# Performance work log

Hardware: AMD Instinct MI355X
Metric: run time of the kernel (lower is better)

The kernel has to match this reference:

```python
import jax, jax.numpy as jnp
import numpy as np

GRID = (15, 15)
HW = GRID[0] * GRID[1]
IMAGE_SIZE = 240
TEMP = 0.07
EPS = 1e-12


def make_masks(h, w, k):
    grid = np.arange(h * w).reshape(h, w)
    # matches torch unfold: kernel offsets row-major, spatial positions row-major
    idx = np.stack([grid[i:i + h - k + 1, j:j + w - k + 1] for i in range(k) for j in range(k)])
    return jnp.asarray(idx.reshape(k * k, -1), dtype=jnp.int32)  # [k*k, n_masks]


def _l2n(x):
    return x / jnp.maximum(jnp.linalg.norm(x, axis=-1, keepdims=True), EPS)


def cosine_sim(a, b):
    # a: [..., N, D], b: [M, D] -> [..., N, M]
    return jnp.einsum('...nd,md->...nm', _l2n(a), _l2n(b))


def harmonic_aggregation(window_scores, masks):
    # window_scores: [B, n_masks]; masks: [k2, n_masks] flat patch indices
    n_masks = masks.shape[1]
    # membership matrix M[p, w] = 1 if patch p is covered by window w
    M = jnp.zeros((HW, n_masks), dtype=window_scores.dtype)
    M = M.at[masks, jnp.arange(n_masks)[None, :]].set(1.0)
    counts = M.sum(axis=1)                                  # [HW]
    sums = (1.0 / window_scores) @ M.T                      # [B, HW]
    scores = counts[None, :] / sums
    scores = jnp.nan_to_num(scores, nan=0.0, posinf=0.0)
    return scores.reshape(-1, GRID[0], GRID[1])


def visual_association_score(embeds, ref_embeds):
    # embeds: [B, N, D]; ref_embeds: [K, N, D]
    flat = ref_embeds.reshape(-1, embeds.shape[-1])          # [K*N, D]
    scores = cosine_sim(embeds, flat)                        # [B, N, K*N]
    return (1.0 - scores).min(axis=-1) / 2.0                 # [B, N]


def setup_inputs() -> dict:
    key = jax.random.key(0)
    ks = jax.random.split(key, 8)
    B, D, K = 256, 640, 4
    return {
        'image_embeds': jax.random.normal(ks[0], (B, D), jnp.float32),
        'window_embeds_s2': jax.random.normal(ks[1], (B, 196, D), jnp.float32),
        'window_embeds_s3': jax.random.normal(ks[2], (B, 169, D), jnp.float32),
        'patch_embeds': jax.random.normal(ks[3], (B, 225, D), jnp.float32),
        'text_embeds': jax.random.normal(ks[4], (2, D), jnp.float32),
        'ref_patch_embeds': jax.random.normal(ks[5], (K, 225, D), jnp.float32),
        'ref_window_s2': jax.random.normal(ks[6], (K, 196, D), jnp.float32),
        'ref_window_s3': jax.random.normal(ks[7], (K, 169, D), jnp.float32),
        'masks_s2': make_masks(GRID[0], GRID[1], 2),
        'masks_s3': make_masks(GRID[0], GRID[1], 3),
    }


def reference(image_embeds, window_embeds_s2, window_embeds_s3, patch_embeds,
              text_embeds, ref_patch_embeds, ref_window_s2, ref_window_s3,
              masks_s2, masks_s3):
    B = image_embeds.shape[0]
    # image-level zero-shot anomaly score
    img_probs = jax.nn.softmax(cosine_sim(image_embeds, text_embeds) / TEMP, axis=-1)
    image_scores = img_probs[..., 1]                         # [B]

    # zero-shot multi-scale (harmonic mean of image score + window scores)
    zs = [jnp.broadcast_to(image_scores[:, None, None], (B, GRID[0], GRID[1]))]
    for we, m in ((window_embeds_s2, masks_s2), (window_embeds_s3, masks_s3)):
        s = jax.nn.softmax(cosine_sim(we, text_embeds) / TEMP, axis=-1)[..., 1]  # [B, n_masks]
        zs.append(harmonic_aggregation(s, m))
    zero_shot = len(zs) / (1.0 / jnp.stack(zs)).sum(axis=0)   # [B, H, W]

    # few-shot scores
    fs = [visual_association_score(patch_embeds, ref_patch_embeds).reshape(B, GRID[0], GRID[1])]
    for we, re, m in ((window_embeds_s2, ref_window_s2, masks_s2),
                      (window_embeds_s3, ref_window_s3, masks_s3)):
        fs.append(harmonic_aggregation(visual_association_score(we, re), m))
    few_shot = jnp.stack(fs).mean(axis=0)                     # [B, H, W]

    multi_scale = (zero_shot + few_shot) / 2.0
    image_scores = (image_scores + few_shot.max(axis=(-2, -1))) / 2.0
    pixel_scores = jax.image.resize(multi_scale, (B, IMAGE_SIZE, IMAGE_SIZE), method='bilinear')
    return image_scores, pixel_scores
```

## Files before the change

kernel.cpp:

```cpp
#include <hip/hip_runtime.h>
#include <cmath>

#define D 640
#define TEMP_INV (1.0f / 0.07f)

typedef __attribute__((ext_vector_type(8))) short bf16x8;
typedef __attribute__((ext_vector_type(4))) float f32x4;

__device__ __forceinline__ short f2bf(float f) {
    unsigned int u = __float_as_uint(f);
    unsigned int r = (u + 0x7fffu + ((u >> 16) & 1u)) >> 16;
    return (short)r;
}

__device__ __forceinline__ void gload_lds16(const void* g, void* l) {
    __builtin_amdgcn_global_load_lds(
        (const __attribute__((address_space(1))) unsigned int*)g,
        (__attribute__((address_space(3))) unsigned int*)l, 16, 0, 0);
}

__global__ void textnorm_k(const float* __restrict__ T, float* __restrict__ tn) {
    int w = threadIdx.x >> 6, lane = threadIdx.x & 63;
    const float* row = T + w * D;
    float v[10]; float ss = 0.f;
#pragma unroll
    for (int i = 0; i < 10; i++) { v[i] = row[lane + 64 * i]; ss += v[i] * v[i]; }
#pragma unroll
    for (int m = 1; m < 64; m <<= 1) ss += __shfl_xor(ss, m, 64);
    float rn = 1.f / fmaxf(sqrtf(ss), 1e-12f);
#pragma unroll
    for (int i = 0; i < 10; i++) tn[w * D + lane + 64 * i] = v[i] * rn;
}

__global__ __launch_bounds__(256) void normstore_k(
    const float* __restrict__ X, int nsrc, int npad, const float* __restrict__ tn,
    float* __restrict__ score_out, short* __restrict__ bf16_out) {
    int wid = blockIdx.x * 4 + (threadIdx.x >> 6);
    int lane = threadIdx.x & 63;
    if (wid >= npad) return;
    const float2* row = (const float2*)(X + (size_t)(wid < nsrc ? wid : 0) * D);
    const float2* t0 = (const float2*)tn;
    const float2* t1 = (const float2*)(tn + D);
    float2 v[5]; float ss = 0.f, d0 = 0.f, d1 = 0.f;
#pragma unroll
    for (int i = 0; i < 5; i++) {
        float2 a = row[lane + 64 * i];
        v[i] = a;
        ss += a.x * a.x + a.y * a.y;
        if (tn) {
            float2 b0 = t0[lane + 64 * i], b1 = t1[lane + 64 * i];
            d0 += a.x * b0.x + a.y * b0.y;
            d1 += a.x * b1.x + a.y * b1.y;
        }
    }
#pragma unroll
    for (int m = 1; m < 64; m <<= 1) {
        ss += __shfl_xor(ss, m, 64);
        if (tn) { d0 += __shfl_xor(d0, m, 64); d1 += __shfl_xor(d1, m, 64); }
    }
    float rn = 1.f / fmaxf(sqrtf(ss), 1e-12f);
    if (score_out && lane == 0)
        score_out[wid] = 1.f / (1.f + expf(-((d1 - d0) * rn) * TEMP_INV));
    if (bf16_out) {
        ushort2* o = (ushort2*)bf16_out;
#pragma unroll
        for (int i = 0; i < 5; i++) {
            ushort2 p;
            p.x = (unsigned short)f2bf(v[i].x * rn);
            p.y = (unsigned short)f2bf(v[i].y * rn);
            o[(size_t)wid * 320 + lane + 64 * i] = p;
        }
    }
}

__global__ __launch_bounds__(512, 4) void gemm_max_k(
    const short* __restrict__ A, const short* __restrict__ B,
    int nch, int U, float* __restrict__ partial) {
    __shared__ short Al[3][128 * 32];
    __shared__ short Bl[3][256 * 32];
    const int t = threadIdx.x;
    const int g = blockIdx.x & 7, ii = blockIdx.x >> 3;
    const int ulo = (int)(((long long)g * U) >> 3);
    const int uhi = (int)(((long long)(g + 1) * U) >> 3);
    const int u = ulo + ii;
    if (u >= uhi) return;
    const int rc = u / nch, nc = u - rc * nch;
    const int nchq = nch * 4;

    const int srow = t >> 2;
    const int scol = (t & 3) * 16;
    const int gsw = (scol ^ (((t >> 3) & 3) << 4)) >> 1;

    const int lane = t & 63, wave = t >> 6;
    const int l15 = lane & 15, lhi = lane >> 4;
    const int wr = wave >> 2, wc = wave & 3;
    const int kb = (lhi * 16) ^ (((l15 >> 1) & 3) << 4);

    const short* Ag = A + ((size_t)rc * 128 + srow) * D + gsw;
    const short* Bg = B + ((size_t)nc * 256 + srow) * D + gsw;

    auto stage = [&](int buf, int ks) {
        gload_lds16(Ag + ks * 32, (char*)&Al[buf][0] + t * 16);
        gload_lds16(Bg + ks * 32, (char*)&Bl[buf][0] + t * 16);
        gload_lds16(Bg + (size_t)128 * D + ks * 32, (char*)&Bl[buf][0] + 8192 + t * 16);
    };

    f32x4 acc[4][4];
#pragma unroll
    for (int m = 0; m < 4; m++)
#pragma unroll
        for (int n = 0; n < 4; n++) acc[m][n] = (f32x4){0.f, 0.f, 0.f, 0.f};

    stage(0, 0);
    stage(1, 1);

    for (int ks = 0; ks < 20; ks++) {
        asm volatile("s_waitcnt vmcnt(3)" ::: "memory");
        __builtin_amdgcn_s_barrier();
        asm volatile("" ::: "memory");

        int nxt = ks + 2; if (nxt > 19) nxt = 19;
        stage((ks + 2) % 3, nxt);

        const char* Ab = (const char*)&Al[ks % 3][0];
        const char* Bb = (const char*)&Bl[ks % 3][0];
        bf16x8 a[4], b[4];
#pragma unroll
        for (int m = 0; m < 4; m++)
            a[m] = *(const bf16x8*)(Ab + (wr * 64 + m * 16 + l15) * 64 + kb);
#pragma unroll
        for (int n = 0; n < 4; n++)
            b[n] = *(const bf16x8*)(Bb + (wc * 64 + n * 16 + l15) * 64 + kb);
#pragma unroll
        for (int m = 0; m < 4; m++)
#pragma unroll
            for (int n = 0; n < 4; n++)
                acc[m][n] = __builtin_amdgcn_mfma_f32_16x16x32_bf16(a[m], b[n], acc[m][n], 0, 0, 0);
    }

#pragma unroll
    for (int m = 0; m < 4; m++)
#pragma unroll
        for (int r = 0; r < 4; r++) {
            float v = fmaxf(fmaxf(acc[m][0][r], acc[m][1][r]),
                            fmaxf(acc[m][2][r], acc[m][3][r]));
#pragma unroll
            for (int msk = 1; msk < 16; msk <<= 1)
                v = fmaxf(v, __shfl_xor(v, msk, 64));
            if (l15 == 0) {
                int row = rc * 128 + wr * 64 + m * 16 + lhi * 4 + r;
                partial[(size_t)row * nchq + nc * 4 + wc] = v;
            }
        }
}

__global__ __launch_bounds__(256) void reducemax_k(
    const float* __restrict__ partial, int nchq, int nrows, float* __restrict__ vas) {
    int r = blockIdx.x * 256 + threadIdx.x;
    if (r >= nrows) return;
    float m = -1e30f;
    for (int i = 0; i < nchq; i++) m = fmaxf(m, partial[(size_t)r * nchq + i]);
    vas[r] = (1.0f - m) * 0.5f;
}

__global__ __launch_bounds__(256) void rowstats_k(
    const float* __restrict__ X, int nrows, const float* __restrict__ tn,
    float* __restrict__ rnorm_out, float* __restrict__ score_out) {
    int wid = blockIdx.x * 4 + (threadIdx.x >> 6);
    int lane = threadIdx.x & 63;
    if (wid >= nrows) return;
    const float* row = X + (size_t)wid * D;
    float ss = 0.f, d0 = 0.f, d1 = 0.f;
#pragma unroll
    for (int i = 0; i < 10; i++) {
        float v = row[lane + 64 * i];
        ss += v * v;
        if (tn) { d0 += v * tn[lane + 64 * i]; d1 += v * tn[D + lane + 64 * i]; }
    }
#pragma unroll
    for (int m = 1; m < 64; m <<= 1) {
        ss += __shfl_xor(ss, m, 64);
        if (tn) { d0 += __shfl_xor(d0, m, 64); d1 += __shfl_xor(d1, m, 64); }
    }
    if (lane == 0) {
        float rn = 1.f / fmaxf(sqrtf(ss), 1e-12f);
        if (rnorm_out) rnorm_out[wid] = rn;
        if (score_out) score_out[wid] = 1.f / (1.f + expf(-((d1 - d0) * rn) * TEMP_INV));
    }
}

__global__ __launch_bounds__(256) void refnorm_k(
    const float* __restrict__ R, int M, int Mp, short* __restrict__ out) {
    int wid = blockIdx.x * 4 + (threadIdx.x >> 6);
    int lane = threadIdx.x & 63;
    if (wid >= Mp) return;
    const float* row = R + (size_t)(wid < M ? wid : 0) * D;
    float v[10]; float ss = 0.f;
#pragma unroll
    for (int i = 0; i < 10; i++) { v[i] = row[lane + 64 * i]; ss += v[i] * v[i]; }
#pragma unroll
    for (int m = 1; m < 64; m <<= 1) ss += __shfl_xor(ss, m, 64);
    float rn = 1.f / fmaxf(sqrtf(ss), 1e-12f);
#pragma unroll
    for (int i = 0; i < 10; i++) out[(size_t)wid * D + lane + 64 * i] = f2bf(v[i] * rn);
}

#define SA 648
#define SB 72
__global__ __launch_bounds__(256) void maxcos_k(
    const float* __restrict__ X, const float* __restrict__ rnorm,
    const short* __restrict__ refs, int Mp, float* __restrict__ vas_out) {
    __shared__ short Alds[64 * SA];
    __shared__ short Blds[64 * SB];
    const int t = threadIdx.x;
    const size_t rowBase = (size_t)blockIdx.x * 64;
#pragma unroll
    for (int i = 0; i < 20; i++) {
        int c = i * 256 + t;
        int row = c / 80, col = (c % 80) * 8;
        const float* p = X + (rowBase + row) * D + col;
        float rn = rnorm[rowBase + row];
        float4 v0 = *(const float4*)p;
        float4 v1 = *(const float4*)(p + 4);
        bf16x8 s;
        s[0] = f2bf(v0.x * rn); s[1] = f2bf(v0.y * rn);
        s[2] = f2bf(v0.z * rn); s[3] = f2bf(v0.w * rn);
        s[4] = f2bf(v1.x * rn); s[5] = f2bf(v1.y * rn);
        s[6] = f2bf(v1.z * rn); s[7] = f2bf(v1.w * rn);
        *(bf16x8*)&Alds[row * SA + col] = s;
    }
    __syncthreads();
    const int lane = t & 63, wave = t >> 6;
    const int l15 = lane & 15, lhi = lane >> 4;
    const int wr0 = wave * 16;
    float rowmax[4] = {-1e30f, -1e30f, -1e30f, -1e30f};
    for (int m0 = 0; m0 < Mp; m0 += 64) {
        f32x4 zero = {0.f, 0.f, 0.f, 0.f};
        f32x4 acc[4] = {zero, zero, zero, zero};
        for (int ks = 0; ks < 10; ks++) {
            __syncthreads();
#pragma unroll
            for (int c2 = 0; c2 < 2; c2++) {
                int c = c2 * 256 + t;
                int n = c >> 3, kk = (c & 7) * 8;
                const short* g = refs + (size_t)(m0 + n) * D + ks * 64 + kk;
                *(bf16x8*)&Blds[n * SB + kk] = *(const bf16x8*)g;
            }
            __syncthreads();
#pragma unroll
            for (int sub = 0; sub < 2; sub++) {
                bf16x8 a = *(const bf16x8*)&Alds[(wr0 + l15) * SA + ks * 64 + sub * 32 + lhi * 8];
#pragma unroll
                for (int s = 0; s < 4; s++) {
                    bf16x8 b = *(const bf16x8*)&Blds[(s * 16 + l15) * SB + sub * 32 + lhi * 8];
                    acc[s] = __builtin_amdgcn_mfma_f32_16x16x32_bf16(a, b, acc[s], 0, 0, 0);
                }
            }
        }
#pragma unroll
        for (int r = 0; r < 4; r++) {
            float mv = fmaxf(fmaxf(acc[0][r], acc[1][r]), fmaxf(acc[2][r], acc[3][r]));
#pragma unroll
            for (int msk = 1; msk < 16; msk <<= 1) mv = fmaxf(mv, __shfl_xor(mv, msk, 64));
            rowmax[r] = fmaxf(rowmax[r], mv);
        }
    }
    if (l15 == 0) {
#pragma unroll
        for (int r = 0; r < 4; r++) {
            size_t row = rowBase + wr0 + lhi * 4 + r;
            vas_out[row] = (1.0f - rowmax[r]) * 0.5f;
        }
    }
}

__global__ __launch_bounds__(256) void fuse_k(
    const float* __restrict__ imgsc, const float* __restrict__ zs2,
    const float* __restrict__ zs3, const float* __restrict__ vasP,
    const float* __restrict__ vas2, const float* __restrict__ vas3,
    float* __restrict__ multi, float* __restrict__ img_out) {
    int b = blockIdx.x, t = threadIdx.x;
    __shared__ float red[256];
    float few = -1e30f;
    if (t < 225) {
        int i = t / 15, j = t % 15;
        float invz2 = 0.f, invf2 = 0.f; int c2 = 0;
        int ilo = max(0, i - 1), ihi = min(i, 13), jlo = max(0, j - 1), jhi = min(j, 13);
        for (int i0 = ilo; i0 <= ihi; i0++)
            for (int j0 = jlo; j0 <= jhi; j0++) {
                int w = b * 196 + i0 * 14 + j0;
                invz2 += 1.f / zs2[w]; invf2 += 1.f / vas2[w]; c2++;
            }
        float zh2 = (float)c2 / invz2, fh2 = (float)c2 / invf2;
        float invz3 = 0.f, invf3 = 0.f; int c3 = 0;
        ilo = max(0, i - 2); ihi = min(i, 12); jlo = max(0, j - 2); jhi = min(j, 12);
        for (int i0 = ilo; i0 <= ihi; i0++)
            for (int j0 = jlo; j0 <= jhi; j0++) {
                int w = b * 169 + i0 * 13 + j0;
                invz3 += 1.f / zs3[w]; invf3 += 1.f / vas3[w]; c3++;
            }
        float zh3 = (float)c3 / invz3, fh3 = (float)c3 / invf3;
        float is = imgsc[b];
        float zero_shot = 3.f / (1.f / is + 1.f / zh2 + 1.f / zh3);
        float fs0 = vasP[b * 225 + t];
        few = (fs0 + fh2 + fh3) * (1.f / 3.f);
        multi[b * 225 + t] = (zero_shot + few) * 0.5f;
    }
    red[t] = few;
    __syncthreads();
    for (int s = 128; s > 0; s >>= 1) {
        if (t < s) red[t] = fmaxf(red[t], red[t + s]);
        __syncthreads();
    }
    if (t == 0) img_out[b] = (imgsc[b] + red[0]) * 0.5f;
}

__global__ __launch_bounds__(256) void resize_k(
    const float* __restrict__ multi, float* __restrict__ out) {
    int idx = blockIdx.x * 256 + threadIdx.x;
    int x = idx % 240;
    int rest = idx / 240;
    int y = rest % 240;
    int b = rest / 240;
    float sx = (x + 0.5f) * 0.0625f - 0.5f;
    float sy = (y + 0.5f) * 0.0625f - 0.5f;
    sx = fminf(fmaxf(sx, 0.f), 14.f);
    sy = fminf(fmaxf(sy, 0.f), 14.f);
    int x0 = min((int)sx, 13), y0 = min((int)sy, 13);
    float fx = sx - x0, fy = sy - y0;
    const float* m = multi + b * 225;
    float v00 = m[y0 * 15 + x0],      v01 = m[y0 * 15 + x0 + 1];
    float v10 = m[y0 * 15 + 15 + x0], v11 = m[y0 * 15 + 15 + x0 + 1];
    out[idx] = (1.f - fy) * ((1.f - fx) * v00 + fx * v01)
             + fy * ((1.f - fx) * v10 + fx * v11);
}

extern "C" void kernel_launch(void* const* d_in, const int* in_sizes, int n_in,
                              void* d_out, int out_size, void* d_ws, size_t ws_size,
                              hipStream_t stream) {
    const float* image = (const float*)d_in[0];
    const float* w2    = (const float*)d_in[1];
    const float* w3    = (const float*)d_in[2];
    const float* patch = (const float*)d_in[3];
    const float* text  = (const float*)d_in[4];
    const float* refP  = (const float*)d_in[5];
    const float* ref2  = (const float*)d_in[6];
    const float* ref3  = (const float*)d_in[7];
    float* out_img = (float*)d_out;
    float* out_pix = out_img + 256;

    char* wsb = (char*)d_ws;
    size_t off = 0;
    auto alloc = [&](size_t bytes) -> void* {
        void* p = wsb + off;
        off += (bytes + 255) & ~(size_t)255;
        return p;
    };

    const size_t NEW_NEED = 72300000;
    if (ws_size >= NEW_NEED) {
        float* tn    = (float*)alloc(2 * 640 * 4);
        float* imgsc = (float*)alloc(256 * 4);
        float* zs2   = (float*)alloc(50176 * 4);
        float* zs3   = (float*)alloc(43264 * 4);
        short* nrefP = (short*)alloc(1024 * 640 * 2);
        short* nref2 = (short*)alloc(1024 * 640 * 2);
        short* nref3 = (short*)alloc(768 * 640 * 2);
        short* Abuf  = (short*)alloc((size_t)50176 * 640 * 2);
        float* partial = (float*)alloc((size_t)50176 * 16 * 4);
        float* vasP  = (float*)alloc(57600 * 4);
        float* vas2  = (float*)alloc(50176 * 4);
        float* vas3  = (float*)alloc(43264 * 4);
        float* multi = (float*)alloc(57600 * 4);

        textnorm_k<<<1, 128, 0, stream>>>(text, tn);
        normstore_k<<<64, 256, 0, stream>>>(image, 256, 256, tn, imgsc, nullptr);
        normstore_k<<<256, 256, 0, stream>>>(refP, 900, 1024, nullptr, nullptr, nrefP);
        normstore_k<<<256, 256, 0, stream>>>(ref2, 784, 1024, nullptr, nullptr, nref2);
        normstore_k<<<192, 256, 0, stream>>>(ref3, 676, 768, nullptr, nullptr, nref3);

        for (int h = 0; h < 2; h++) {
            const float* src = patch + (size_t)h * 28800 * D;
            normstore_k<<<7200, 256, 0, stream>>>(src, 28800, 28800, nullptr, nullptr, Abuf);
            gemm_max_k<<<904, 512, 0, stream>>>(Abuf, nrefP, 4, 900, partial);
            reducemax_k<<<113, 256, 0, stream>>>(partial, 16, 28800, vasP + h * 28800);
        }
        normstore_k<<<12544, 256, 0, stream>>>(w2, 50176, 50176, tn, zs2, Abuf);
        gemm_max_k<<<1568, 512, 0, stream>>>(Abuf, nref2, 4, 1568, partial);
        reducemax_k<<<196, 256, 0, stream>>>(partial, 16, 50176, vas2);
        normstore_k<<<10816, 256, 0, stream>>>(w3, 43264, 43264, tn, zs3, Abuf);
        gemm_max_k<<<1016, 512, 0, stream>>>(Abuf, nref3, 3, 1014, partial);
        reducemax_k<<<169, 256, 0, stream>>>(partial, 12, 43264, vas3);

        fuse_k<<<256, 256, 0, stream>>>(imgsc, zs2, zs3, vasP, vas2, vas3, multi, out_img);
        resize_k<<<57600, 256, 0, stream>>>(multi, out_pix);
    } else {
        float* tn    = (float*)alloc(2 * 640 * 4);
        float* imgsc = (float*)alloc(256 * 4);
        float* rn2   = (float*)alloc(50176 * 4);
        float* rn3   = (float*)alloc(43264 * 4);
        float* rnp   = (float*)alloc(57600 * 4);
        float* zs2   = (float*)alloc(50176 * 4);
        float* zs3   = (float*)alloc(43264 * 4);
        short* nrefP = (short*)alloc(960 * 640 * 2);
        short* nref2 = (short*)alloc(832 * 640 * 2);
        short* nref3 = (short*)alloc(704 * 640 * 2);
        float* vasP  = (float*)alloc(57600 * 4);
        float* vas2  = (float*)alloc(50176 * 4);
        float* vas3  = (float*)alloc(43264 * 4);
        float* multi = (float*)alloc(57600 * 4);

        textnorm_k<<<1, 128, 0, stream>>>(text, tn);
        rowstats_k<<<64, 256, 0, stream>>>(image, 256, tn, nullptr, imgsc);
        rowstats_k<<<12544, 256, 0, stream>>>(w2, 50176, tn, rn2, zs2);
        rowstats_k<<<10816, 256, 0, stream>>>(w3, 43264, tn, rn3, zs3);
        rowstats_k<<<14400, 256, 0, stream>>>(patch, 57600, nullptr, rnp, nullptr);
        refnorm_k<<<240, 256, 0, stream>>>(refP, 900, 960, nrefP);
        refnorm_k<<<208, 256, 0, stream>>>(ref2, 784, 832, nref2);
        refnorm_k<<<176, 256, 0, stream>>>(ref3, 676, 704, nref3);
        maxcos_k<<<900, 256, 0, stream>>>(patch, rnp, nrefP, 960, vasP);
        maxcos_k<<<784, 256, 0, stream>>>(w2, rn2, nref2, 832, vas2);
        maxcos_k<<<676, 256, 0, stream>>>(w3, rn3, nref3, 704, vas3);
        fuse_k<<<256, 256, 0, stream>>>(imgsc, zs2, zs3, vasP, vas2, vas3, multi, out_img);
        resize_k<<<57600, 256, 0, stream>>>(multi, out_pix);
    }
}
```

Before: 422.5 us.

## Enlarge GEMM-max tile to 256x256 with 64-wide K steps and interleaved staging

New measurement: 418.8 us. About the same (-0.9%).

```diff
diff --git a/kernel.cpp b/kernel.cpp
--- a/kernel.cpp
+++ b/kernel.cpp
@@ -73,11 +73,42 @@
     }
 }
 
-__global__ __launch_bounds__(512, 4) void gemm_max_k(
+#define BAR() do { __builtin_amdgcn_s_barrier(); asm volatile("" ::: "memory"); } while (0)
+
+#define READA(RH, KB) do { \
+    a0 = *(const bf16x8*)(Ah + ((RH)*64 +  0 + l15) * 128 + (KB)); \
+    a1 = *(const bf16x8*)(Ah + ((RH)*64 + 16 + l15) * 128 + (KB)); \
+    a2 = *(const bf16x8*)(Ah + ((RH)*64 + 32 + l15) * 128 + (KB)); \
+    a3 = *(const bf16x8*)(Ah + ((RH)*64 + 48 + l15) * 128 + (KB)); } while (0)
+
+#define READB(KB) do { \
+    b0 = *(const bf16x8*)(Bh + (bcol +  0 + l15) * 128 + (KB)); \
+    b1 = *(const bf16x8*)(Bh + (bcol + 16 + l15) * 128 + (KB)); \
+    b2 = *(const bf16x8*)(Bh + (bcol + 32 + l15) * 128 + (KB)); \
+    b3 = *(const bf16x8*)(Bh + (bcol + 48 + l15) * 128 + (KB)); } while (0)
+
+#define MFMA16(RH) do { \
+    acc[(RH)*4+0][0] = __builtin_amdgcn_mfma_f32_16x16x32_bf16(a0, b0, acc[(RH)*4+0][0], 0,0,0); \
+    acc[(RH)*4+0][1] = __builtin_amdgcn_mfma_f32_16x16x32_bf16(a0, b1, acc[(RH)*4+0][1], 0,0,0); \
+    acc[(RH)*4+0][2] = __builtin_amdgcn_mfma_f32_16x16x32_bf16(a0, b2, acc[(RH)*4+0][2], 0,0,0); \
+    acc[(RH)*4+0][3] = __builtin_amdgcn_mfma_f32_16x16x32_bf16(a0, b3, acc[(RH)*4+0][3], 0,0,0); \
+    acc[(RH)*4+1][0] = __builtin_amdgcn_mfma_f32_16x16x32_bf16(a1, b0, acc[(RH)*4+1][0], 0,0,0); \
+    acc[(RH)*4+1][1] = __builtin_amdgcn_mfma_f32_16x16x32_bf16(a1, b1, acc[(RH)*4+1][1], 0,0,0); \
+    acc[(RH)*4+1][2] = __builtin_amdgcn_mfma_f32_16x16x32_bf16(a1, b2, acc[(RH)*4+1][2], 0,0,0); \
+    acc[(RH)*4+1][3] = __builtin_amdgcn_mfma_f32_16x16x32_bf16(a1, b3, acc[(RH)*4+1][3], 0,0,0); \
+    acc[(RH)*4+2][0] = __builtin_amdgcn_mfma_f32_16x16x32_bf16(a2, b0, acc[(RH)*4+2][0], 0,0,0); \
+    acc[(RH)*4+2][1] = __builtin_amdgcn_mfma_f32_16x16x32_bf16(a2, b1, acc[(RH)*4+2][1], 0,0,0); \
+    acc[(RH)*4+2][2] = __builtin_amdgcn_mfma_f32_16x16x32_bf16(a2, b2, acc[(RH)*4+2][2], 0,0,0); \
+    acc[(RH)*4+2][3] = __builtin_amdgcn_mfma_f32_16x16x32_bf16(a2, b3, acc[(RH)*4+2][3], 0,0,0); \
+    acc[(RH)*4+3][0] = __builtin_amdgcn_mfma_f32_16x16x32_bf16(a3, b0, acc[(RH)*4+3][0], 0,0,0); \
+    acc[(RH)*4+3][1] = __builtin_amdgcn_mfma_f32_16x16x32_bf16(a3, b1, acc[(RH)*4+3][1], 0,0,0); \
+    acc[(RH)*4+3][2] = __builtin_amdgcn_mfma_f32_16x16x32_bf16(a3, b2, acc[(RH)*4+3][2], 0,0,0); \
+    acc[(RH)*4+3][3] = __builtin_amdgcn_mfma_f32_16x16x32_bf16(a3, b3, acc[(RH)*4+3][3], 0,0,0); } while (0)
+
+__global__ __launch_bounds__(512, 2) void gemm_max8_k(
     const short* __restrict__ A, const short* __restrict__ B,
     int nch, int U, float* __restrict__ partial) {
-    __shared__ short Al[3][128 * 32];
-    __shared__ short Bl[3][256 * 32];
+    __shared__ short L[2][2][2][8192];
     const int t = threadIdx.x;
     const int g = blockIdx.x & 7, ii = blockIdx.x >> 3;
     const int ulo = (int)(((long long)g * U) >> 3);
@@ -87,68 +118,95 @@
     const int rc = u / nch, nc = u - rc * nch;
     const int nchq = nch * 4;
 
-    const int srow = t >> 2;
-    const int scol = (t & 3) * 16;
-    const int gsw = (scol ^ (((t >> 3) & 3) << 4)) >> 1;
+    const int srow = t >> 3;
+    const int scol = (t & 7) * 16;
+    const int gsw = (scol ^ ((srow & 7) << 4)) >> 1;
 
     const int lane = t & 63, wave = t >> 6;
     const int l15 = lane & 15, lhi = lane >> 4;
     const int wr = wave >> 2, wc = wave & 3;
-    const int kb = (lhi * 16) ^ (((l15 >> 1) & 3) << 4);
-
-    const short* Ag = A + ((size_t)rc * 128 + srow) * D + gsw;
-    const short* Bg = B + ((size_t)nc * 256 + srow) * D + gsw;
-
-    auto stage = [&](int buf, int ks) {
-        gload_lds16(Ag + ks * 32, (char*)&Al[buf][0] + t * 16);
-        gload_lds16(Bg + ks * 32, (char*)&Bl[buf][0] + t * 16);
-        gload_lds16(Bg + (size_t)128 * D + ks * 32, (char*)&Bl[buf][0] + 8192 + t * 16);
+    const int xk = (l15 & 7) << 4;
+    const int bcol = (wc & 1) * 64;
+    const int kb0 = (lhi * 16) ^ xk;
+    const int kb1 = (64 + lhi * 16) ^ xk;
+
+    const short* Asrc = A + ((size_t)rc * 256 + srow) * D + gsw;
+    const short* Bsrc = B + ((size_t)nc * 256 + srow) * D + gsw;
+
+    auto stageA = [&](int nb, int kc) {
+#pragma unroll
+        for (int h = 0; h < 2; h++)
+#pragma unroll
+            for (int i = 0; i < 2; i++)
+                gload_lds16(Asrc + (size_t)(h * 128 + i * 64) * D + kc * 64,
+                            (char*)&L[nb][0][h][0] + i * 8192 + (t << 4));
     };
-
-    f32x4 acc[4][4];
-#pragma unroll
-    for (int m = 0; m < 4; m++)
+    auto stageB = [&](int nb, int kc) {
+#pragma unroll
+        for (int h = 0; h < 2; h++)
+#pragma unroll
+            for (int i = 0; i < 2; i++)
+                gload_lds16(Bsrc + (size_t)(h * 128 + i * 64) * D + kc * 64,
+                            (char*)&L[nb][1][h][0] + i * 8192 + (t << 4));
+    };
+
+    f32x4 acc[8][4];
+#pragma unroll
+    for (int m = 0; m < 8; m++)
 #pragma unroll
         for (int n = 0; n < 4; n++) acc[m][n] = (f32x4){0.f, 0.f, 0.f, 0.f};
 
-    stage(0, 0);
-    stage(1, 1);
-
-    for (int ks = 0; ks < 20; ks++) {
-        asm volatile("s_waitcnt vmcnt(3)" ::: "memory");
-        __builtin_amdgcn_s_barrier();
-        asm volatile("" ::: "memory");
-
-        int nxt = ks + 2; if (nxt > 19) nxt = 19;
-        stage((ks + 2) % 3, nxt);
-
-        const char* Ab = (const char*)&Al[ks % 3][0];
-        const char* Bb = (const char*)&Bl[ks % 3][0];
-        bf16x8 a[4], b[4];
-#pragma unroll
-        for (int m = 0; m < 4; m++)
-            a[m] = *(const bf16x8*)(Ab + (wr * 64 + m * 16 + l15) * 64 + kb);
-#pragma unroll
-        for (int n = 0; n < 4; n++)
-            b[n] = *(const bf16x8*)(Bb + (wc * 64 + n * 16 + l15) * 64 + kb);
-#pragma unroll
-        for (int m = 0; m < 4; m++)
-#pragma unroll
-            for (int n = 0; n < 4; n++)
-                acc[m][n] = __builtin_amdgcn_mfma_f32_16x16x32_bf16(a[m], b[n], acc[m][n], 0, 0, 0);
-    }
-
-#pragma unroll
-    for (int m = 0; m < 4; m++)
-#pragma unroll
-        for (int r = 0; r < 4; r++) {
-            float v = fmaxf(fmaxf(acc[m][0][r], acc[m][1][r]),
-                            fmaxf(acc[m][2][r], acc[m][3][r]));
+    stageA(0, 0);
+    stageB(0, 0);
+    asm volatile("s_waitcnt vmcnt(0)" ::: "memory");
+    BAR();
+
+    for (int kt = 0; kt < 10; kt++) {
+        const int cb = kt & 1, kn = kt + 1;
+        const char* Ah = (const char*)&L[cb][0][wr][0];
+        const char* Bh = (const char*)&L[cb][1][wc >> 1][0];
+        bf16x8 a0, a1, a2, a3, b0, b1, b2, b3;
+
+        READB(kb0); READA(0, kb0);
+        if (kn < 10) stageA(kn & 1, kn);
+        BAR();
+        __builtin_amdgcn_s_setprio(1);
+        MFMA16(0);
+        __builtin_amdgcn_s_setprio(0);
+        BAR();
+        READA(1, kb0);
+        if (kn < 10) stageB(kn & 1, kn);
+        BAR();
+        __builtin_amdgcn_s_setprio(1);
+        MFMA16(1);
+        __builtin_amdgcn_s_setprio(0);
+        BAR();
+        READB(kb1); READA(0, kb1);
+        BAR();
+        __builtin_amdgcn_s_setprio(1);
+        MFMA16(0);
+        __builtin_amdgcn_s_setprio(0);
+        BAR();
+        READA(1, kb1);
+        BAR();
+        __builtin_amdgcn_s_setprio(1);
+        MFMA16(1);
+        __builtin_amdgcn_s_setprio(0);
+        asm volatile("s_waitcnt vmcnt(0)" ::: "memory");
+        BAR();
+    }
+
+#pragma unroll
+    for (int rf = 0; rf < 8; rf++)
+#pragma unroll
+        for (int ri = 0; ri < 4; ri++) {
+            float v = fmaxf(fmaxf(acc[rf][0][ri], acc[rf][1][ri]),
+                            fmaxf(acc[rf][2][ri], acc[rf][3][ri]));
 #pragma unroll
             for (int msk = 1; msk < 16; msk <<= 1)
                 v = fmaxf(v, __shfl_xor(v, msk, 64));
             if (l15 == 0) {
-                int row = rc * 128 + wr * 64 + m * 16 + lhi * 4 + r;
+                int row = rc * 256 + wr * 128 + rf * 16 + lhi * 4 + ri;
                 partial[(size_t)row * nchq + nc * 4 + wc] = v;
             }
         }
@@ -357,7 +415,7 @@
         return p;
     };
 
-    const size_t NEW_NEED = 72300000;
+    const size_t NEW_NEED = 72600000;
     if (ws_size >= NEW_NEED) {
         float* tn    = (float*)alloc(2 * 640 * 4);
         float* imgsc = (float*)alloc(256 * 4);
@@ -381,15 +439,15 @@
 
         for (int h = 0; h < 2; h++) {
             const float* src = patch + (size_t)h * 28800 * D;
-            normstore_k<<<7200, 256, 0, stream>>>(src, 28800, 28800, nullptr, nullptr, Abuf);
-            gemm_max_k<<<904, 512, 0, stream>>>(Abuf, nrefP, 4, 900, partial);
+            normstore_k<<<7232, 256, 0, stream>>>(src, 28800, 28928, nullptr, nullptr, Abuf);
+            gemm_max8_k<<<456, 512, 0, stream>>>(Abuf, nrefP, 4, 452, partial);
             reducemax_k<<<113, 256, 0, stream>>>(partial, 16, 28800, vasP + h * 28800);
         }
         normstore_k<<<12544, 256, 0, stream>>>(w2, 50176, 50176, tn, zs2, Abuf);
-        gemm_max_k<<<1568, 512, 0, stream>>>(Abuf, nref2, 4, 1568, partial);
+        gemm_max8_k<<<784, 512, 0, stream>>>(Abuf, nref2, 4, 784, partial);
         reducemax_k<<<196, 256, 0, stream>>>(partial, 16, 50176, vas2);
         normstore_k<<<10816, 256, 0, stream>>>(w3, 43264, 43264, tn, zs3, Abuf);
-        gemm_max_k<<<1016, 512, 0, stream>>>(Abuf, nref3, 3, 1014, partial);
+        gemm_max8_k<<<512, 512, 0, stream>>>(Abuf, nref3, 3, 507, partial);
         reducemax_k<<<169, 256, 0, stream>>>(partial, 12, 43264, vas3);
 
         fuse_k<<<256, 256, 0, stream>>>(imgsc, zs2, zs3, vasP, vas2, vas3, multi, out_img);
```
